# Kernel optimization log

Hardware: AMD Instinct MI355X
Metric: run time of the kernel (lower is better)

The kernel has to match this reference:

```python
import jax, jax.numpy as jnp
import numpy as np

NV, NA, T, FD, C, E = 192, 64, 128, 1024, 128, 262144
SPK = 3
N = (NV + NA) * T  # 32768 total graph nodes
NEG = -1e30


def _seg_max(msg, dst, mask):
    # masked scatter-max; PyG fills segments with no messages with 0
    m = jnp.where(mask[:, None], msg, NEG)
    out = jax.ops.segment_max(m, dst, num_segments=N)
    return jnp.where(out > NEG * 0.5, out, 0.0)


def _edge_conv(x, src, dst, mask, W1, b1, W2, b2):
    # EdgeConv: max_j MLP(cat[x_i, x_j - x_i])
    xi = x[dst]
    h = jnp.concatenate([xi, x[src] - xi], axis=-1)  # [E, 2C]
    h = jax.nn.relu(h @ W1 + b1) @ W2 + b2
    return _seg_max(h, dst, mask)


def _sage_conv(x, src, dst, mask, Wl, bl, Wr):
    # SAGEConv: lin_l(mean_j x_j) + lin_r(x_i), lin_r has no bias
    mf = mask.astype(x.dtype)
    s = jax.ops.segment_sum(x[src] * mf[:, None], dst, num_segments=N)
    cnt = jax.ops.segment_sum(mf, dst, num_segments=N)
    mean = s / jnp.maximum(cnt, 1.0)[:, None]
    return mean @ Wl + bl + x @ Wr


def setup_inputs():
    ks = jax.random.split(jax.random.key(0), 24)
    s = 0.05
    vals = jnp.array([-3, -2, -1, 0, 1, 3], jnp.int32)
    return {
        "x_visual": jax.random.normal(ks[0], (NV, T, FD), jnp.float32),
        "x_audio": jax.random.normal(ks[1], (NA, T, FD), jnp.float32),
        "W011": jax.random.normal(ks[2], (FD, C)) * s, "b011": jnp.zeros((C,)),
        "W012": jax.random.normal(ks[3], (FD, C)) * s, "b012": jnp.zeros((C,)),
        "ecA_W1": jax.random.normal(ks[4], (2 * C, C)) * s, "ecA_b1": jnp.zeros((C,)),
        "ecA_W2": jax.random.normal(ks[5], (C, C)) * s, "ecA_b2": jnp.zeros((C,)),
        "ec1_W1": jax.random.normal(ks[6], (2 * C, C)) * s, "ec1_b1": jnp.zeros((C,)),
        "ec1_W2": jax.random.normal(ks[7], (C, C)) * s, "ec1_b2": jnp.zeros((C,)),
        "ec2_W1": jax.random.normal(ks[8], (2 * C, C)) * s, "ec2_b1": jnp.zeros((C,)),
        "ec2_W2": jax.random.normal(ks[9], (C, C)) * s, "ec2_b2": jnp.zeros((C,)),
        "ec3_W1": jax.random.normal(ks[10], (2 * C, C)) * s, "ec3_b1": jnp.zeros((C,)),
        "ec3_W2": jax.random.normal(ks[11], (C, C)) * s, "ec3_b2": jnp.zeros((C,)),
        "sage_Wl": jax.random.normal(ks[12], (C, C)) * s, "sage_bl": jnp.zeros((C,)),
        "sage_Wr": jax.random.normal(ks[13], (C, C)) * s,
        "fc_W": jax.random.normal(ks[14], (C, 1)) * s, "fc_b": jnp.zeros((1,)),
        "edge_index": jax.random.randint(ks[15], (2, E), 0, N, dtype=jnp.int32),
        "edge_attr": vals[jax.random.randint(ks[16], (E,), 0, 6)],
        "speakers": SPK,
    }


def reference(x_visual, x_audio, W011, b011, W012, b012,
              ecA_W1, ecA_b1, ecA_W2, ecA_b2,
              ec1_W1, ec1_b1, ec1_W2, ec1_b2,
              ec2_W1, ec2_b1, ec2_W2, ec2_b2,
              ec3_W1, ec3_b1, ec3_W2, ec3_b2,
              sage_Wl, sage_bl, sage_Wr, fc_W, fc_b,
              edge_index, edge_attr, speakers):
    xv = x_visual @ W011 + b011          # [NV, T, C]
    xa = x_audio @ W012 + b012           # [NA, T, C]
    x = jnp.concatenate([xv, xa], axis=0).reshape(-1, C)  # [N, C]
    src, dst = edge_index[0], edge_index[1]
    m_audio = edge_attr == -2
    m_vpa = edge_attr == -3
    m_acv = edge_attr == 3
    m1 = (edge_attr >= 0) & (edge_attr <= 1)
    m2 = (edge_attr <= 0) & (edge_attr >= -1)
    m3 = jnp.abs(edge_attr) <= 1
    # Visual_Add_Audio_GNN: max-aggregate (x_i + x_j)
    xa_g = jax.nn.relu(_seg_max(x[dst] + x[src], dst, m_vpa))
    a = jax.nn.relu(_edge_conv(xa_g, src, dst, m_audio, ecA_W1, ecA_b1, ecA_W2, ecA_b2))
    a_res = a @ fc_W + fc_b              # [N, 1] per-node audio scores
    # Audio_Weight_Add_Visual_GNN: sum-aggregate (w_j * x_j + x_i)
    wmsg = jnp.where(m_acv[:, None], a_res[src] * x[src] + x[dst], 0.0)
    xv2 = jax.nn.relu(jax.ops.segment_sum(wmsg, dst, num_segments=N))

    def branch(mask, W1, b1, W2, b2):
        h = jax.nn.relu(_edge_conv(xv2, src, dst, mask, W1, b1, W2, b2))
        return jax.nn.relu(_sage_conv(h, src, dst, mask, sage_Wl, sage_bl, sage_Wr))

    xo = (branch(m1, ec1_W1, ec1_b1, ec1_W2, ec1_b2)
          + branch(m2, ec2_W1, ec2_b1, ec2_W2, ec2_b2)
          + branch(m3, ec3_W1, ec3_b1, ec3_W2, ec3_b2))
    # gather main-speaker visual nodes
    idx = (jnp.arange(0, NV * T, speakers * T)[:, None] + jnp.arange(T)).reshape(-1)
    return xo[idx]
```

## Files before the change

### kernel.cpp

```cpp
#include <hip/hip_runtime.h>
#include <cstdint>
#include <cstddef>

#define NVv 192
#define NAa 64
#define TT 128
#define FDd 1024
#define CCc 128
#define EEe 262144
#define NNn 32768

typedef _Float16 f16x8 __attribute__((ext_vector_type(8)));
typedef float f32x4 __attribute__((ext_vector_type(4)));

#define CAP0 65536
#define CAP1 65536
#define CAP2 65536
#define CAP3 98304
#define CAP4 98304
#define CAP5 147456
#define ARENA_TOTAL (CAP0+CAP1+CAP2+CAP3+CAP4+CAP5)

__device__ __forceinline__ void eval_masks(int a, bool m[6]) {
    m[0] = (a == -3); m[1] = (a == -2); m[2] = (a == 3);
    m[3] = (a >= 0) & (a <= 1);
    m[4] = (a >= -1) & (a <= 0);
    m[5] = (a >= -1) & (a <= 1);
}

__global__ __launch_bounds__(256) void k_zero(float* __restrict__ p) {
    size_t i = (size_t)blockIdx.x * 1024 + (size_t)threadIdx.x * 4;
    *(float4*)(p + i) = make_float4(0.f, 0.f, 0.f, 0.f);
}

__global__ __launch_bounds__(256) void k_zero_need(
    const int* __restrict__ histj, const int* __restrict__ basej,
    float* __restrict__ AH)
{
    int col = threadIdx.x & 127, sub = threadIdx.x >> 7;
    for (int d = blockIdx.x * 2 + sub; d < NNn; d += gridDim.x * 2) {
        int c = histj[d];
        bool need;
        if (c == 0) need = true;
        else {
            int b = basej[d], e = b + c;
            need = ((b & 63) == 0) || ((e & 63) == 0) || ((b >> 6) != ((e - 1) >> 6));
        }
        if (need) AH[(size_t)d * 128 + col] = 0.f;
    }
}

__global__ __launch_bounds__(256) void k_wprep_big(
    const float* __restrict__ W011, const float* __restrict__ W012,
    _Float16* __restrict__ dst)
{
    int idx = blockIdx.x * 256 + threadIdx.x;
    int which = idx >> 17;
    int r = idx & 131071;
    int n = r >> 10, k = r & 1023;
    const float* src = which ? W012 : W011;
    dst[idx] = (_Float16)src[k * 128 + n];
}

struct WSmall { const float* p[14]; };

__global__ __launch_bounds__(256) void k_wprep_small(WSmall ws, _Float16* __restrict__ dst)
{
    int idx = blockIdx.x * 256 + threadIdx.x;
    int seg = idx >> 14;
    int r = idx & 16383;
    int n = r >> 7, k = r & 127;
    const float* src = ws.p[seg];
    float v = src[k * 128 + n];
    if (seg < 12 && (seg % 3) == 0) v -= src[16384 + k * 128 + n];
    dst[idx] = (_Float16)v;
}

__global__ __launch_bounds__(256) void k_hist(
    const int* __restrict__ attr, const int* __restrict__ edst,
    int* __restrict__ hist)
{
    int e = blockIdx.x * 256 + threadIdx.x;
    int a = attr[e], d = edst[e];
    bool m[6]; eval_masks(a, m);
#pragma unroll
    for (int j = 0; j < 6; ++j)
        if (m[j]) atomicAdd(&hist[j * NNn + d], 1);
}

__global__ __launch_bounds__(256) void k_scan_a(
    const int* __restrict__ hist, int* __restrict__ base, int* __restrict__ bsum)
{
    __shared__ int wsum[4];
    int bid = blockIdx.x;
    int idx = bid * 256 + threadIdx.x;
    int tid = threadIdx.x, lane = tid & 63, wv = tid >> 6;
    int v = hist[idx];
    int x = v;
#pragma unroll
    for (int off = 1; off < 64; off <<= 1) {
        int y = __shfl_up(x, off, 64);
        if (lane >= off) x += y;
    }
    if (lane == 63) wsum[wv] = x;
    __syncthreads();
    int add = 0;
    for (int w = 0; w < wv; ++w) add += wsum[w];
    base[idx] = add + x - v;
    if (tid == 255) bsum[bid] = add + x;
}

__global__ __launch_bounds__(384) void k_scan_b(int* __restrict__ bsum, int* __restrict__ cnts)
{
    int wv = threadIdx.x >> 6;
    int lane = threadIdx.x & 63;
    int run = 0;
#pragma unroll
    for (int c0 = 0; c0 < 128; c0 += 64) {
        int v = bsum[wv * 128 + c0 + lane];
        int x = v;
#pragma unroll
        for (int off = 1; off < 64; off <<= 1) {
            int y = __shfl_up(x, off, 64);
            if (lane >= off) x += y;
        }
        bsum[wv * 128 + c0 + lane] = run + (x - v);
        run += __shfl(x, 63, 64);
    }
    if (lane == 0) cnts[wv] = run;
}

__global__ __launch_bounds__(256) void k_scan_c(int* __restrict__ base, const int* __restrict__ bsum)
{
    base[blockIdx.x * 256 + threadIdx.x] += bsum[blockIdx.x];
}

__global__ __launch_bounds__(256) void k_fill(
    const int* __restrict__ esrc, const int* __restrict__ edst,
    const int* __restrict__ attr, const int* __restrict__ base,
    int* __restrict__ fill, int2* __restrict__ arena)
{
    int e = blockIdx.x * 256 + threadIdx.x;
    int a = attr[e];
    int s = esrc[e], d = edst[e];
    bool m[6]; eval_masks(a, m);
    const int caps[6] = {CAP0, CAP1, CAP2, CAP3, CAP4, CAP5};
    const int offs[6] = {0, CAP0, CAP0+CAP1, CAP0+CAP1+CAP2,
                         CAP0+CAP1+CAP2+CAP3, CAP0+CAP1+CAP2+CAP3+CAP4};
#pragma unroll
    for (int j = 0; j < 6; ++j) {
        if (m[j]) {
            int pos = base[j * NNn + d] + atomicAdd(&fill[j * NNn + d], 1);
            if (pos < caps[j]) arena[offs[j] + pos] = make_int2(s, d);
        }
    }
}

__global__ __launch_bounds__(512) void k_proj(
    const float* __restrict__ xv, const float* __restrict__ xa,
    const _Float16* __restrict__ BTv, const _Float16* __restrict__ BTa,
    float* __restrict__ Pp0, float* __restrict__ Pp1)
{
    __shared__ _Float16 Bl[128][136];
    const int tid = threadIdx.x, wave = tid >> 6, lane = tid & 63;
    const int tile = blockIdx.x >> 1, kh = blockIdx.x & 1;
    const float* A; const _Float16* BT; int mbase, obase;
    if (tile < 192) { A = xv; BT = BTv; mbase = tile * 128; obase = mbase; }
    else { A = xa; BT = BTa; mbase = (tile - 192) * 128; obase = 24576 + mbase; }
    float* Pout = kh ? Pp1 : Pp0;
    const int kbase = kh * 512;

    const int mrow = mbase + wave * 16 + (lane & 15);
    const int fk   = (lane >> 4) * 8;
    f32x4 acc[8];
#pragma unroll
    for (int i = 0; i < 8; ++i) acc[i] = (f32x4){0,0,0,0};

    f16x8 af[4];
#pragma unroll
    for (int t4 = 0; t4 < 4; ++t4) {
        const float* asrc = A + (size_t)mrow * 1024 + kbase + t4 * 32 + fk;
        float4 a0 = *(const float4*)asrc;
        float4 a1 = *(const float4*)(asrc + 4);
        af[t4] = (f16x8){ (_Float16)a0.x, (_Float16)a0.y, (_Float16)a0.z, (_Float16)a0.w,
                          (_Float16)a1.x, (_Float16)a1.y, (_Float16)a1.z, (_Float16)a1.w };
    }

    for (int kc = 0; kc < 4; ++kc) {
        __syncthreads();
#pragma unroll
        for (int it = 0; it < 4; ++it) {
            int c = it * 512 + tid;
            int n = c >> 4, koff = (c & 15) * 8;
            *(f16x8*)&Bl[n][koff] =
                *(const f16x8*)(BT + (size_t)n * 1024 + kbase + kc * 128 + koff);
        }
        __syncthreads();
        f16x8 nf[4];
        if (kc < 3) {
#pragma unroll
            for (int t4 = 0; t4 < 4; ++t4) {
                const float* asrc = A + (size_t)mrow * 1024 + kbase + (kc + 1) * 128 + t4 * 32 + fk;
                float4 a0 = *(const float4*)asrc;
                float4 a1 = *(const float4*)(asrc + 4);
                nf[t4] = (f16x8){ (_Float16)a0.x, (_Float16)a0.y, (_Float16)a0.z, (_Float16)a0.w,
                                  (_Float16)a1.x, (_Float16)a1.y, (_Float16)a1.z, (_Float16)a1.w };
            }
        }
#pragma unroll
        for (int t4 = 0; t4 < 4; ++t4)
#pragma unroll
            for (int nt = 0; nt < 8; ++nt) {
                f16x8 bf = *(const f16x8*)&Bl[nt * 16 + (lane & 15)][t4 * 32 + fk];
                acc[nt] = __builtin_amdgcn_mfma_f32_16x16x32_f16(af[t4], bf, acc[nt], 0, 0, 0);
            }
#pragma unroll
        for (int t4 = 0; t4 < 4; ++t4) af[t4] = nf[t4];
    }
    __syncthreads();
    const int cbase = lane & 15, rloc = (lane >> 4) * 4;
    const int wgrp = wave & 3;
    float* Hsf = (float*)&Bl[0][0] + (size_t)wgrp * 16 * 132;
#pragma unroll
    for (int grp = 0; grp < 2; ++grp) {
        if ((wave >> 2) == grp) {
#pragma unroll
            for (int nt = 0; nt < 8; ++nt) {
                int c2 = nt * 16 + cbase;
#pragma unroll
                for (int rr = 0; rr < 4; ++rr)
                    Hsf[(rloc + rr) * 132 + c2] = acc[nt][rr];
            }
#pragma unroll
            for (int it = 0; it < 8; ++it) {
                int id = it * 64 + lane;
                int row = id >> 5, off = (id & 31) * 4;
                float4 v = *(float4*)&Hsf[row * 132 + off];
                *(float4*)&Pout[(size_t)(obase + wave * 16 + row) * 128 + off] = v;
            }
        }
        __syncthreads();
    }
}

__global__ __launch_bounds__(256) void k_reduce(
    const float* __restrict__ Pp0, const float* __restrict__ Pp1,
    const float* __restrict__ b011, const float* __restrict__ b012,
    float* __restrict__ X)
{
    size_t f = (size_t)blockIdx.x * 256 + threadIdx.x;
    size_t i = f * 4;
    int col = (int)(i & 127);
    int row = (int)(i >> 7);
    const float* bias = (row < 24576) ? b011 : b012;
    float4 a = *(const float4*)(Pp0 + i);
    float4 b = *(const float4*)(Pp1 + i);
    float4 bb = *(const float4*)(bias + col);
    float4 o = make_float4(a.x + b.x + bb.x, a.y + b.y + bb.y,
                           a.z + b.z + bb.z, a.w + b.w + bb.w);
    *(float4*)(X + i) = o;
}

__global__ __launch_bounds__(256) void k_pv(
    const float* __restrict__ A,
    const _Float16* __restrict__ BT1, const float* __restrict__ b1,
    const _Float16* __restrict__ BT2,
    _Float16* __restrict__ P, _Float16* __restrict__ V)
{
    __shared__ _Float16 Bl1[128][136];
    __shared__ _Float16 Bl2[128][136];
    __shared__ float bb[128];
    const int tid = threadIdx.x, wave = tid >> 6, lane = tid & 63;
    const int r0 = blockIdx.x * 64 + wave * 16;

    const int fk = (lane >> 4) * 8;
    const int mrow = blockIdx.x * 64 + wave * 16 + (lane & 15);
    float4 a0[4], a1[4];
#pragma unroll
    for (int t4 = 0; t4 < 4; ++t4) {
        const float* asrc = A + (size_t)mrow * 128 + t4 * 32 + fk;
        a0[t4] = *(const float4*)asrc;
        a1[t4] = *(const float4*)(asrc + 4);
    }
#pragma unroll
    for (int it = 0; it < 8; ++it) {
        int c = it * 256 + tid;
        int n = c >> 4, koff = (c & 15) * 8;
        *(f16x8*)&Bl1[n][koff] = *(const f16x8*)(BT1 + (size_t)n * 128 + koff);
        *(f16x8*)&Bl2[n][koff] = *(const f16x8*)(BT2 + (size_t)n * 128 + koff);
    }
    if (tid < 128) bb[tid] = b1[tid];
    __syncthreads();

    f16x8 af[4];
#pragma unroll
    for (int t4 = 0; t4 < 4; ++t4)
        af[t4] = (f16x8){ (_Float16)a0[t4].x, (_Float16)a0[t4].y, (_Float16)a0[t4].z, (_Float16)a0[t4].w,
                          (_Float16)a1[t4].x, (_Float16)a1[t4].y, (_Float16)a1[t4].z, (_Float16)a1[t4].w };
    f32x4 acc1[8], acc2[8];
#pragma unroll
    for (int i = 0; i < 8; ++i) { acc1[i] = (f32x4){0,0,0,0}; acc2[i] = (f32x4){0,0,0,0}; }
#pragma unroll
    for (int t4 = 0; t4 < 4; ++t4)
#pragma unroll
        for (int nt = 0; nt < 8; ++nt) {
            f16x8 bf1 = *(const f16x8*)&Bl1[nt * 16 + (lane & 15)][t4 * 32 + fk];
            f16x8 bf2 = *(const f16x8*)&Bl2[nt * 16 + (lane & 15)][t4 * 32 + fk];
            acc1[nt] = __builtin_amdgcn_mfma_f32_16x16x32_f16(af[t4], bf1, acc1[nt], 0, 0, 0);
            acc2[nt] = __builtin_amdgcn_mfma_f32_16x16x32_f16(af[t4], bf2, acc2[nt], 0, 0, 0);
        }
    __syncthreads();
    _Float16* Hs = &Bl1[0][0] + (size_t)wave * 16 * 136;
    const int cbase = lane & 15, rloc = (lane >> 4) * 4;
#pragma unroll
    for (int nt = 0; nt < 8; ++nt) {
        int c2 = nt * 16 + cbase;
        float bvv = bb[c2];
#pragma unroll
        for (int rr = 0; rr < 4; ++rr)
            Hs[(rloc + rr) * 136 + c2] = (_Float16)(acc1[nt][rr] + bvv);
    }
#pragma unroll
    for (int it = 0; it < 4; ++it) {
        int id = it * 64 + lane;
        int row = id >> 4, koff = (id & 15) * 8;
        *(f16x8*)&P[(size_t)(r0 + row) * 128 + koff] = *(f16x8*)&Hs[row * 136 + koff];
    }
#pragma unroll
    for (int nt = 0; nt < 8; ++nt) {
        int c2 = nt * 16 + cbase;
#pragma unroll
        for (int rr = 0; rr < 4; ++rr)
            Hs[(rloc + rr) * 136 + c2] = (_Float16)acc2[nt][rr];
    }
#pragma unroll
    for (int it = 0; it < 4; ++it) {
        int id = it * 64 + lane;
        int row = id >> 4, koff = (id & 15) * 8;
        *(f16x8*)&V[(size_t)(r0 + row) * 128 + koff] = *(f16x8*)&Hs[row * 136 + koff];
    }
}

__global__ __launch_bounds__(256, 3) void k_edge_mlp(
    const _Float16* __restrict__ P, const _Float16* __restrict__ V,
    const _Float16* __restrict__ W2T, const float* __restrict__ b2,
    const int2* __restrict__ list, const int* __restrict__ cntp, int cap,
    float* __restrict__ agg)
{
    __shared__ _Float16 Rl[64][136];
    __shared__ _Float16 W2l[128][136];
    __shared__ float b2l[128];
    __shared__ int2 eSD[64];
    __shared__ unsigned char gstart[66];
    __shared__ int gdst[64];
    __shared__ int ngrS;

    int cnt = min(*cntp, cap);
    int ntiles = (cnt + 63) >> 6;
    if ((int)blockIdx.x >= ntiles) return;

    const int tid  = threadIdx.x;
    const int wave = tid >> 6;
    const int lane = tid & 63;

#pragma unroll
    for (int i = 0; i < 8; ++i) {
        int c = tid + i * 256;
        int n = c >> 4, koff = (c & 15) * 8;
        *(f16x8*)&W2l[n][koff] = *(const f16x8*)(W2T + n * 128 + koff);
    }
    if (tid < 128) b2l[tid] = b2[tid];

    const int col   = tid & 127;
    const int half  = tid >> 7;
    const int frow  = wave * 16 + (lane & 15);
    const int fq    = (lane >> 4) * 8;
    const int rbase = wave * 16 + (lane >> 4) * 4;
    const int cbase = lane & 15;
    const int rrow  = tid >> 4;
    const int rch   = (tid & 15) * 8;

    for (int t = blockIdx.x; t < ntiles; t += gridDim.x) {
        __syncthreads();
        if (tid < 64) {
            int e = t * 64 + tid;
            eSD[tid] = (e < cnt) ? list[e] : make_int2(0, -1);
        }
        __syncthreads();
        if (tid < 64) {
            int d = eSD[tid].y;
            bool flag = (tid == 0) || (d != eSD[tid - 1].y);
            unsigned long long bm = __ballot(flag);
            int rank = (int)__popcll(bm & ((1ull << tid) - 1ull));
            if (flag) { gstart[rank] = (unsigned char)tid; gdst[rank] = d; }
            if (tid == 0) {
                int ng = (int)__popcll(bm);
                ngrS = ng;
                gstart[ng] = 64;
            }
        }
#pragma unroll
        for (int p = 0; p < 4; ++p) {
            int i = p * 16 + rrow;
            int2 sd = eSD[i];
            f16x8 rv = {0, 0, 0, 0, 0, 0, 0, 0};
            if (sd.y >= 0) {
                f16x8 pv = *(const f16x8*)(P + (size_t)sd.y * 128 + rch);
                f16x8 vv = *(const f16x8*)(V + (size_t)sd.x * 128 + rch);
                rv = pv + vv;
#pragma unroll
                for (int q = 0; q < 8; ++q)
                    rv[q] = (rv[q] > (_Float16)0.f) ? rv[q] : (_Float16)0.f;
            }
            *(f16x8*)&Rl[i][rch] = rv;
        }
        __syncthreads();

        f32x4 acc[8];
#pragma unroll
        for (int i = 0; i < 8; ++i) acc[i] = (f32x4){0,0,0,0};
#pragma unroll
        for (int t4 = 0; t4 < 4; ++t4) {
            f16x8 af = *(const f16x8*)&Rl[frow][t4 * 32 + fq];
#pragma unroll
            for (int nt = 0; nt < 8; ++nt) {
                f16x8 bf = *(const f16x8*)&W2l[nt * 16 + (lane & 15)][t4 * 32 + fq];
                acc[nt] = __builtin_amdgcn_mfma_f32_16x16x32_f16(af, bf, acc[nt], 0, 0, 0);
            }
        }
        __syncthreads();
#pragma unroll
        for (int nt = 0; nt < 8; ++nt) {
            int c2 = nt * 16 + cbase;
            float bv = b2l[c2];
#pragma unroll
            for (int rr = 0; rr < 4; ++rr)
                Rl[rbase + rr][c2] = (_Float16)fmaxf(acc[nt][rr] + bv, 0.f);
        }
        __syncthreads();
        int ng = ngrS;
        for (int g = half; g < ng; g += 2) {
            int s = gstart[g], e = gstart[g + 1];
            int d = gdst[g];
            if (d < 0) continue;
            float m = 0.f;
            for (int i = s; i < e; ++i)
                m = fmaxf(m, (float)Rl[i][col]);
            size_t o = (size_t)d * 128 + col;
            if (s == 0 || e == 64)
                atomicMax((unsigned int*)&agg[o], __float_as_uint(m));
            else
                agg[o] = m;
        }
    }
}

__global__ __launch_bounds__(256) void k_csr_vpa(
    const float* __restrict__ X, const int2* __restrict__ list,
    const int* __restrict__ base, const int* __restrict__ cntarr, int cap,
    float* __restrict__ S)
{
    int col = threadIdx.x & 127;
    int sub = threadIdx.x >> 7;
    for (int d = blockIdx.x * 2 + sub; d < NNn; d += gridDim.x * 2) {
        int c = cntarr[d];
        float v = 0.f;
        if (c > 0) {
            int b = base[d];
            int end = min(b + c, cap);
            float mx = -3.0e38f;
            for (int i = b; i < end; ++i)
                mx = fmaxf(mx, X[(size_t)list[i].x * 128 + col]);
            v = fmaxf(X[(size_t)d * 128 + col] + mx, 0.f);
        }
        S[(size_t)d * 128 + col] = v;
    }
}

__global__ __launch_bounds__(256) void k_csr_acv(
    const float* __restrict__ X, const float* __restrict__ ares,
    const int2* __restrict__ list,
    const int* __restrict__ base, const int* __restrict__ cntarr, int cap,
    float* __restrict__ S)
{
    int col = threadIdx.x & 127;
    int sub = threadIdx.x >> 7;
    for (int d = blockIdx.x * 2 + sub; d < NNn; d += gridDim.x * 2) {
        int c = cntarr[d];
        float v = 0.f;
        if (c > 0) {
            int b = base[d];
            int end = min(b + c, cap);
            float s = 0.f;
            for (int i = b; i < end; ++i) {
                int sr = list[i].x;
                s += ares[sr] * X[(size_t)sr * 128 + col];
            }
            v = fmaxf(s + (float)c * X[(size_t)d * 128 + col], 0.f);
        }
        S[(size_t)d * 128 + col] = v;
    }
}

__global__ __launch_bounds__(256) void k_csr_meanc(
    const float* __restrict__ AH, const int2* __restrict__ list,
    const int* __restrict__ basej, const int* __restrict__ histj, int cap,
    const int* __restrict__ spk, int ntarg,
    float* __restrict__ S1c, float* __restrict__ AHc)
{
    int col = threadIdx.x & 127;
    int sub = threadIdx.x >> 7;
    int step = spk[0] * TT;
    for (int ci = blockIdx.x * 2 + sub; ci < ntarg; ci += gridDim.x * 2) {
        int d = (ci >> 7) * step + (ci & 127);
        int c = histj[d];
        float v = 0.f;
        if (c > 0) {
            int b = basej[d];
            int end = min(b + c, cap);
            float s = 0.f;
            for (int i = b; i < end; ++i)
                s += AH[(size_t)list[i].x * 128 + col];
            v = s / (float)c;
        }
        S1c[(size_t)ci * 128 + col] = v;
        AHc[(size_t)ci * 128 + col] = AH[(size_t)d * 128 + col];
    }
}

__global__ __launch_bounds__(256) void k_fc(
    const float* __restrict__ A, const float* __restrict__ W,
    const float* __restrict__ b, float* __restrict__ ares)
{
    int node = blockIdx.x * 4 + (threadIdx.x >> 6);
    int lane = threadIdx.x & 63;
    const float* row = A + (size_t)node * 128;
    float v = row[lane] * W[lane] + row[lane + 64] * W[lane + 64];
#pragma unroll
    for (int off = 32; off > 0; off >>= 1) v += __shfl_down(v, off, 64);
    if (lane == 0) ares[node] = v + b[0];
}

__global__ __launch_bounds__(256) void k_sage_out(
    const float* __restrict__ S1c, const float* __restrict__ AHc,
    const _Float16* __restrict__ WlT, const _Float16* __restrict__ WrT,
    const float* __restrict__ bl, float* __restrict__ out, int ntarg)
{
    __shared__ _Float16 Al[64][40];
    __shared__ _Float16 Bl[128][40];
    const int tid  = threadIdx.x;
    const int wave = tid >> 6;
    const int lane = tid & 63;
    const int m0   = blockIdx.x * 64;

    f32x4 accB[8], accO[8];
#pragma unroll
    for (int i = 0; i < 8; ++i) { accB[i] = (f32x4){0,0,0,0}; accO[i] = (f32x4){0,0,0,0}; }

    const int ar = tid >> 2;
    const int ak = (tid & 3) * 8;
    const int fr = wave * 16 + (lane & 15);
    const int fk = (lane >> 4) * 8;
    const int rbase = wave * 16 + (lane >> 4) * 4;
    const int cbase = lane & 15;

    for (int seg = 0; seg < 6; ++seg) {
        int b = seg >> 1, which = seg & 1;
        const float* A = (which ? AHc : S1c) + (size_t)b * ntarg * 128;
        const _Float16* BT = which ? WrT : WlT;
        for (int k0 = 0; k0 < 128; k0 += 32) {
            __syncthreads();
            const float* asrc = A + (size_t)(m0 + ar) * 128 + (k0 + ak);
            float4 a0 = *(const float4*)asrc;
            float4 a1 = *(const float4*)(asrc + 4);
            f16x8 av = { (_Float16)a0.x, (_Float16)a0.y, (_Float16)a0.z, (_Float16)a0.w,
                         (_Float16)a1.x, (_Float16)a1.y, (_Float16)a1.z, (_Float16)a1.w };
            *(f16x8*)&Al[ar][ak] = av;
#pragma unroll
            for (int i = 0; i < 2; ++i) {
                int c = tid + i * 256;
                int n = c >> 2, koff = (c & 3) * 8;
                *(f16x8*)&Bl[n][koff] = *(const f16x8*)(BT + (size_t)n * 128 + k0 + koff);
            }
            __syncthreads();
            f16x8 af = *(const f16x8*)&Al[fr][fk];
#pragma unroll
            for (int nt = 0; nt < 8; ++nt) {
                f16x8 bf = *(const f16x8*)&Bl[nt * 16 + (lane & 15)][fk];
                accB[nt] = __builtin_amdgcn_mfma_f32_16x16x32_f16(af, bf, accB[nt], 0, 0, 0);
            }
        }
        if (which) {
#pragma unroll
            for (int nt = 0; nt < 8; ++nt) {
                int col = nt * 16 + cbase;
                float bv = bl[col];
#pragma unroll
                for (int rr = 0; rr < 4; ++rr) {
                    accO[nt][rr] += fmaxf(accB[nt][rr] + bv, 0.f);
                    accB[nt][rr] = 0.f;
                }
            }
        }
    }
#pragma unroll
    for (int nt = 0; nt < 8; ++nt) {
        int col = nt * 16 + cbase;
#pragma unroll
        for (int rr = 0; rr < 4; ++rr)
            out[(size_t)(m0 + rbase + rr) * 128 + col] = accO[nt][rr];
    }
}

extern "C" void kernel_launch(void* const* d_in, const int* in_sizes, int n_in,
                              void* d_out, int out_size, void* d_ws, size_t ws_size,
                              hipStream_t stream)
{
    (void)in_sizes; (void)n_in; (void)ws_size;
    const float* xv   = (const float*)d_in[0];
    const float* xa   = (const float*)d_in[1];
    const float* W011 = (const float*)d_in[2];
    const float* b011 = (const float*)d_in[3];
    const float* W012 = (const float*)d_in[4];
    const float* b012 = (const float*)d_in[5];
    const float* ecW1[4] = {(const float*)d_in[6],  (const float*)d_in[10],
                            (const float*)d_in[14], (const float*)d_in[18]};
    const float* ecb1[4] = {(const float*)d_in[7],  (const float*)d_in[11],
                            (const float*)d_in[15], (const float*)d_in[19]};
    const float* ecW2[4] = {(const float*)d_in[8],  (const float*)d_in[12],
                            (const float*)d_in[16], (const float*)d_in[20]};
    const float* ecb2[4] = {(const float*)d_in[9],  (const float*)d_in[13],
                            (const float*)d_in[17], (const float*)d_in[21]};
    const float* sageWl = (const float*)d_in[22];
    const float* sagebl = (const float*)d_in[23];
    const float* sageWr = (const float*)d_in[24];
    const float* fcW    = (const float*)d_in[25];
    const float* fcb    = (const float*)d_in[26];
    const int*   esrc   = (const int*)d_in[27];
    const int*   edst   = esrc + EEe;
    const int*   attr   = (const int*)d_in[28];
    const int*   spk    = (const int*)d_in[29];
    float* out = (float*)d_out;
    const int ntarg = out_size >> 7;

    const size_t NC = (size_t)NNn * CCc;
    float* ws   = (float*)d_ws;
    float* X    = ws;
    float* S1   = ws + 1 * NC;
    float* AH   = ws + 2 * NC;
    float* XV2  = ws + 3 * NC;
    float* AHc  = ws + 4 * NC;
    _Float16* P16 = (_Float16*)(ws + 5 * NC);
    _Float16* V16 = P16 + NC;
    float* ARES = ws + 6 * NC;
    int*   cnts = (int*)(ARES + NNn);
    int*   bsum = cnts + 16;
    int*   hist = bsum + 1024;
    int*   fill = hist + 6 * NNn;
    int*   base = fill + 6 * NNn;
    int2*  arena = (int2*)(base + 6 * NNn);
    _Float16* WT = (_Float16*)(arena + ARENA_TOTAL);

    const int offs[6] = {0, CAP0, CAP0+CAP1, CAP0+CAP1+CAP2,
                         CAP0+CAP1+CAP2+CAP3, CAP0+CAP1+CAP2+CAP3+CAP4};
    const int caps[6] = {CAP0, CAP1, CAP2, CAP3, CAP4, CAP5};

    const _Float16* W011T = WT;
    const _Float16* W012T = WT + 131072;
    const _Float16* WTs   = WT + 262144;
    const _Float16* WlT   = WTs + 12 * 16384;
    const _Float16* WrT   = WTs + 13 * 16384;

    k_wprep_big<<<1024, 256, 0, stream>>>(W011, W012, WT);
    WSmall wsm;
    for (int i = 0; i < 4; ++i) {
        wsm.p[3*i + 0] = ecW1[i];
        wsm.p[3*i + 1] = ecW1[i] + 16384;
        wsm.p[3*i + 2] = ecW2[i];
    }
    wsm.p[12] = sageWl; wsm.p[13] = sageWr;
    k_wprep_small<<<896, 256, 0, stream>>>(wsm, (_Float16*)WTs);
    k_zero<<<(2 * 6 * NNn) / 1024, 256, 0, stream>>>((float*)hist);
    k_hist<<<EEe / 256, 256, 0, stream>>>(attr, edst, hist);
    k_scan_a<<<768, 256, 0, stream>>>(hist, base, bsum);
    k_scan_b<<<1, 384, 0, stream>>>(bsum, cnts);
    k_scan_c<<<768, 256, 0, stream>>>(base, bsum);
    k_fill<<<EEe / 256, 256, 0, stream>>>(esrc, edst, attr, base, fill, arena);

    k_proj<<<512, 512, 0, stream>>>(xv, xa, W011T, W012T, XV2, AH);
    k_reduce<<<(int)(NC / 1024), 256, 0, stream>>>(XV2, AH, b011, b012, X);
    k_csr_vpa<<<2048, 256, 0, stream>>>(X, arena + offs[0], base + 0 * NNn,
                                        hist + 0 * NNn, caps[0], S1);
    k_pv<<<512, 256, 0, stream>>>(S1, WTs, ecb1[0], WTs + 16384, P16, V16);
    k_zero_need<<<2048, 256, 0, stream>>>(hist + 1 * NNn, base + 1 * NNn, AH);
    k_edge_mlp<<<2048, 256, 0, stream>>>(P16, V16, WTs + 2 * 16384, ecb2[0],
                                         arena + offs[1], cnts + 1, caps[1], AH);
    k_fc<<<NNn / 4, 256, 0, stream>>>(AH, fcW, fcb, ARES);
    k_csr_acv<<<2048, 256, 0, stream>>>(X, ARES, arena + offs[2], base + 2 * NNn,
                                        hist + 2 * NNn, caps[2], XV2);
    for (int b = 0; b < 3; ++b) {
        int j = 3 + b;
        const _Float16* Wd = WTs + (3 * (b + 1)) * 16384;
        k_pv<<<512, 256, 0, stream>>>(XV2, Wd, ecb1[b + 1], Wd + 16384, P16, V16);
        k_zero_need<<<2048, 256, 0, stream>>>(hist + j * NNn, base + j * NNn, AH);
        k_edge_mlp<<<2048, 256, 0, stream>>>(P16, V16, Wd + 2 * 16384, ecb2[b + 1],
                                             arena + offs[j], cnts + j, caps[j], AH);
        k_csr_meanc<<<2048, 256, 0, stream>>>(AH, arena + offs[j], base + j * NNn,
                                              hist + j * NNn, caps[j], spk, ntarg,
                                              S1 + (size_t)b * ntarg * 128,
                                              AHc + (size_t)b * ntarg * 128);
    }
    k_sage_out<<<ntarg / 64, 256, 0, stream>>>(S1, AHc, WlT, WrT, sagebl, out, ntarg);
}
```

Measured before the change: 559.9 us.

## Batch AH zeroing into one launch and double-buffer weight tiles in k_proj

Gives each edge-MLP stage its own AH buffer so that all four partial-zeroing passes run in a single launch before the projection, instead of three separate launches interleaved with the pipeline. The projection kernel now double-buffers its weight tile in shared memory, loading the next K chunk while the current one feeds MFMAs, with one barrier per iteration instead of two. This grows the workspace by three node-feature buffers and doubles k_proj shared memory, which may lower occupancy.

```diff
diff --git a/kernel.cpp b/kernel.cpp
--- a/kernel.cpp
+++ b/kernel.cpp
@@ -33,20 +33,27 @@
     *(float4*)(p + i) = make_float4(0.f, 0.f, 0.f, 0.f);
 }
 
-__global__ __launch_bounds__(256) void k_zero_need(
-    const int* __restrict__ histj, const int* __restrict__ basej,
-    float* __restrict__ AH)
+__global__ __launch_bounds__(256) void k_zero4(
+    const int* __restrict__ hist, const int* __restrict__ base,
+    float* __restrict__ AH0, float* __restrict__ AH1,
+    float* __restrict__ AH2, float* __restrict__ AH3)
 {
     int col = threadIdx.x & 127, sub = threadIdx.x >> 7;
+    const int js[4] = {1, 3, 4, 5};
+    float* AHs[4] = {AH0, AH1, AH2, AH3};
     for (int d = blockIdx.x * 2 + sub; d < NNn; d += gridDim.x * 2) {
-        int c = histj[d];
-        bool need;
-        if (c == 0) need = true;
-        else {
-            int b = basej[d], e = b + c;
-            need = ((b & 63) == 0) || ((e & 63) == 0) || ((b >> 6) != ((e - 1) >> 6));
-        }
-        if (need) AH[(size_t)d * 128 + col] = 0.f;
+#pragma unroll
+        for (int jj = 0; jj < 4; ++jj) {
+            int j = js[jj];
+            int c = hist[j * NNn + d];
+            bool need;
+            if (c == 0) need = true;
+            else {
+                int b = base[j * NNn + d], e = b + c;
+                need = ((b & 63) == 0) || ((e & 63) == 0) || ((b >> 6) != ((e - 1) >> 6));
+            }
+            if (need) AHs[jj][(size_t)d * 128 + col] = 0.f;
+        }
     }
 }
 
@@ -161,7 +168,7 @@
     const _Float16* __restrict__ BTv, const _Float16* __restrict__ BTa,
     float* __restrict__ Pp0, float* __restrict__ Pp1)
 {
-    __shared__ _Float16 Bl[128][136];
+    __shared__ _Float16 Bl[2][128][136];
     const int tid = threadIdx.x, wave = tid >> 6, lane = tid & 63;
     const int tile = blockIdx.x >> 1, kh = blockIdx.x & 1;
     const float* A; const _Float16* BT; int mbase, obase;
@@ -176,6 +183,12 @@
 #pragma unroll
     for (int i = 0; i < 8; ++i) acc[i] = (f32x4){0,0,0,0};
 
+#pragma unroll
+    for (int it = 0; it < 4; ++it) {
+        int c = it * 512 + tid;
+        int n = c >> 4, koff = (c & 15) * 8;
+        *(f16x8*)&Bl[0][n][koff] = *(const f16x8*)(BT + (size_t)n * 1024 + kbase + koff);
+    }
     f16x8 af[4];
 #pragma unroll
     for (int t4 = 0; t4 < 4; ++t4) {
@@ -185,19 +198,20 @@
         af[t4] = (f16x8){ (_Float16)a0.x, (_Float16)a0.y, (_Float16)a0.z, (_Float16)a0.w,
                           (_Float16)a1.x, (_Float16)a1.y, (_Float16)a1.z, (_Float16)a1.w };
     }
+    __syncthreads();
 
     for (int kc = 0; kc < 4; ++kc) {
-        __syncthreads();
-#pragma unroll
-        for (int it = 0; it < 4; ++it) {
-            int c = it * 512 + tid;
-            int n = c >> 4, koff = (c & 15) * 8;
-            *(f16x8*)&Bl[n][koff] =
-                *(const f16x8*)(BT + (size_t)n * 1024 + kbase + kc * 128 + koff);
-        }
-        __syncthreads();
+        const int cur = kc & 1;
         f16x8 nf[4];
         if (kc < 3) {
+            const int nxt = cur ^ 1;
+#pragma unroll
+            for (int it = 0; it < 4; ++it) {
+                int c = it * 512 + tid;
+                int n = c >> 4, koff = (c & 15) * 8;
+                *(f16x8*)&Bl[nxt][n][koff] =
+                    *(const f16x8*)(BT + (size_t)n * 1024 + kbase + (kc + 1) * 128 + koff);
+            }
 #pragma unroll
             for (int t4 = 0; t4 < 4; ++t4) {
                 const float* asrc = A + (size_t)mrow * 1024 + kbase + (kc + 1) * 128 + t4 * 32 + fk;
@@ -211,16 +225,18 @@
         for (int t4 = 0; t4 < 4; ++t4)
 #pragma unroll
             for (int nt = 0; nt < 8; ++nt) {
-                f16x8 bf = *(const f16x8*)&Bl[nt * 16 + (lane & 15)][t4 * 32 + fk];
+                f16x8 bf = *(const f16x8*)&Bl[cur][nt * 16 + (lane & 15)][t4 * 32 + fk];
                 acc[nt] = __builtin_amdgcn_mfma_f32_16x16x32_f16(af[t4], bf, acc[nt], 0, 0, 0);
             }
-#pragma unroll
-        for (int t4 = 0; t4 < 4; ++t4) af[t4] = nf[t4];
-    }
-    __syncthreads();
+        if (kc < 3) {
+#pragma unroll
+            for (int t4 = 0; t4 < 4; ++t4) af[t4] = nf[t4];
+        }
+        __syncthreads();
+    }
     const int cbase = lane & 15, rloc = (lane >> 4) * 4;
     const int wgrp = wave & 3;
-    float* Hsf = (float*)&Bl[0][0] + (size_t)wgrp * 16 * 132;
+    float* Hsf = (float*)&Bl[0][0][0] + (size_t)wgrp * 16 * 132;
 #pragma unroll
     for (int grp = 0; grp < 2; ++grp) {
         if ((wave >> 2) == grp) {
@@ -647,12 +663,15 @@
     float* ws   = (float*)d_ws;
     float* X    = ws;
     float* S1   = ws + 1 * NC;
-    float* AH   = ws + 2 * NC;
-    float* XV2  = ws + 3 * NC;
-    float* AHc  = ws + 4 * NC;
-    _Float16* P16 = (_Float16*)(ws + 5 * NC);
+    float* XV2  = ws + 2 * NC;
+    float* AHc  = ws + 3 * NC;
+    float* AH0  = ws + 4 * NC;
+    float* AH1  = ws + 5 * NC;
+    float* AH2  = ws + 6 * NC;
+    float* AH3  = ws + 7 * NC;
+    _Float16* P16 = (_Float16*)(ws + 8 * NC);
     _Float16* V16 = P16 + NC;
-    float* ARES = ws + 6 * NC;
+    float* ARES = ws + 9 * NC;
     int*   cnts = (int*)(ARES + NNn);
     int*   bsum = cnts + 16;
     int*   hist = bsum + 1024;
@@ -660,6 +679,7 @@
     int*   base = fill + 6 * NNn;
     int2*  arena = (int2*)(base + 6 * NNn);
     _Float16* WT = (_Float16*)(arena + ARENA_TOTAL);
+    float* AHb[4] = {AH0, AH1, AH2, AH3};
 
     const int offs[6] = {0, CAP0, CAP0+CAP1, CAP0+CAP1+CAP2,
                          CAP0+CAP1+CAP2+CAP3, CAP0+CAP1+CAP2+CAP3+CAP4};
@@ -686,26 +706,25 @@
     k_scan_b<<<1, 384, 0, stream>>>(bsum, cnts);
     k_scan_c<<<768, 256, 0, stream>>>(base, bsum);
     k_fill<<<EEe / 256, 256, 0, stream>>>(esrc, edst, attr, base, fill, arena);
-
-    k_proj<<<512, 512, 0, stream>>>(xv, xa, W011T, W012T, XV2, AH);
-    k_reduce<<<(int)(NC / 1024), 256, 0, stream>>>(XV2, AH, b011, b012, X);
+    k_zero4<<<2048, 256, 0, stream>>>(hist, base, AH0, AH1, AH2, AH3);
+
+    k_proj<<<512, 512, 0, stream>>>(xv, xa, W011T, W012T, S1, XV2);
+    k_reduce<<<(int)(NC / 1024), 256, 0, stream>>>(S1, XV2, b011, b012, X);
     k_csr_vpa<<<2048, 256, 0, stream>>>(X, arena + offs[0], base + 0 * NNn,
                                         hist + 0 * NNn, caps[0], S1);
     k_pv<<<512, 256, 0, stream>>>(S1, WTs, ecb1[0], WTs + 16384, P16, V16);
-    k_zero_need<<<2048, 256, 0, stream>>>(hist + 1 * NNn, base + 1 * NNn, AH);
     k_edge_mlp<<<2048, 256, 0, stream>>>(P16, V16, WTs + 2 * 16384, ecb2[0],
-                                         arena + offs[1], cnts + 1, caps[1], AH);
-    k_fc<<<NNn / 4, 256, 0, stream>>>(AH, fcW, fcb, ARES);
+                                         arena + offs[1], cnts + 1, caps[1], AH0);
+    k_fc<<<NNn / 4, 256, 0, stream>>>(AH0, fcW, fcb, ARES);
     k_csr_acv<<<2048, 256, 0, stream>>>(X, ARES, arena + offs[2], base + 2 * NNn,
                                         hist + 2 * NNn, caps[2], XV2);
     for (int b = 0; b < 3; ++b) {
         int j = 3 + b;
         const _Float16* Wd = WTs + (3 * (b + 1)) * 16384;
         k_pv<<<512, 256, 0, stream>>>(XV2, Wd, ecb1[b + 1], Wd + 16384, P16, V16);
-        k_zero_need<<<2048, 256, 0, stream>>>(hist + j * NNn, base + j * NNn, AH);
         k_edge_mlp<<<2048, 256, 0, stream>>>(P16, V16, Wd + 2 * 16384, ecb2[b + 1],
-                                             arena + offs[j], cnts + j, caps[j], AH);
-        k_csr_meanc<<<2048, 256, 0, stream>>>(AH, arena + offs[j], base + j * NNn,
+                                             arena + offs[j], cnts + j, caps[j], AHb[b + 1]);
+        k_csr_meanc<<<2048, 256, 0, stream>>>(AHb[b + 1], arena + offs[j], base + j * NNn,
                                               hist + j * NNn, caps[j], spk, ntarg,
                                               S1 + (size_t)b * ntarg * 128,
                                               AHc + (size_t)b * ntarg * 128);
```

Measured after the change: 554.4 us. About the same (-1.0%).
